# Kernel tuning notes

Measured on AMD Instinct MI355X. Metric: run time of the kernel, lower is better.

Reference implementation:

```python
import jax, jax.numpy as jnp
import numpy as np

N = 8192          # codeword length (power of 2)
K = 4096          # info bits (rate 1/2)
BS = 8192         # batch of codewords


def _gen_indices(n):
    """Stage-wise gather indices for the Arikan butterfly.
    Row s: position ind_dest XORs with ind_dest + 2**s; all other positions
    gather the sentinel column n, which holds a constant 0 (XOR identity)."""
    nb_stages = int(np.log2(n))
    ind = np.full((nb_stages, n + 1), n, dtype=np.int32)
    for s in range(nb_stages):
        r = np.arange(n // 2)
        ind_dest = r * 2 - (r % (2 ** s))
        ind[s, ind_dest] = ind_dest + 2 ** s
    return ind


def setup_inputs() -> dict:
    key = jax.random.key(0)
    u = jax.random.randint(key, (BS, K), 0, 2).astype(jnp.float32)  # info bits in {0,1}
    frozen_pos = np.arange(N - K)
    info_pos = jnp.asarray(np.setdiff1d(np.arange(N), frozen_pos), dtype=jnp.int32)
    ind_gather = jnp.asarray(_gen_indices(N))  # [log2(N), N+1] int32
    return {"u": u, "info_pos": info_pos, "ind_gather": ind_gather}


def reference(u, info_pos, ind_gather):
    bs = u.shape[0]
    n = ind_gather.shape[1] - 1
    nb_stages = ind_gather.shape[0]
    # scatter info bits into codeword positions (frozen positions stay 0)
    c = jnp.zeros((bs, n), dtype=u.dtype).at[:, info_pos].set(u)
    # append the zero sentinel column used as XOR identity
    x = jnp.concatenate([c, jnp.zeros((bs, 1), dtype=u.dtype)], axis=1)  # [bs, n+1]
    for s in range(nb_stages):  # fixed log2(n) structurally-distinct stages
        x = (x + x[:, ind_gather[s]]) % 2  # XOR on {0,1} bits
    return x[:, :n]
```

## Files before the change

kernel.cpp:

```cpp
#include <hip/hip_runtime.h>


typedef unsigned u32x4 __attribute__((ext_vector_type(4)));

constexpr int ROWS      = 8192;
constexpr int K_QUADS   = 1024;
constexpr int OUT_WORDS = 8192;

__global__ __launch_bounds__(64)
void polar_encode_kernel(const u32x4* __restrict__ u, unsigned* __restrict__ out) {
    __shared__ u32x4 lds[1024];

    const int l   = threadIdx.x;
    const int row = blockIdx.x;

    const u32x4* urow = u + (size_t)row * K_QUADS + (size_t)l * 16;
    u32x4 v[16];
#pragma unroll
    for (int r = 0; r < 16; ++r) v[r] = __builtin_nontemporal_load(&urow[r]);

#pragma unroll
    for (int r = 0; r < 16; ++r) { v[r][0] ^= v[r][1]; v[r][2] ^= v[r][3]; }
#pragma unroll
    for (int r = 0; r < 16; ++r) { v[r][0] ^= v[r][2]; v[r][1] ^= v[r][3]; }
#pragma unroll
    for (int s = 0; s < 4; ++s) {
#pragma unroll
        for (int r = 0; r < 16; ++r) {
            if (!(r & (1 << s))) {
                const int p = r | (1 << s);
                v[r][0] ^= v[p][0]; v[r][1] ^= v[p][1];
                v[r][2] ^= v[p][2]; v[r][3] ^= v[p][3];
            }
        }
    }

    const int swz = l & 15;
#pragma unroll
    for (int r = 0; r < 16; ++r)
        lds[(l << 4) + (r ^ swz)] = v[r];

    __syncthreads();

    const unsigned* ldsw = (const unsigned*)lds;
    const int cbase = l >> 2;
    const int clow  = l & 3;
    unsigned g[64];
#pragma unroll
    for (int j = 0; j < 64; ++j) {
        g[j] = ldsw[(j << 6) + ((cbase ^ (j & 15)) << 2) + clow];
    }

#pragma unroll
    for (int s = 0; s < 6; ++s) {
#pragma unroll
        for (int j = 0; j < 64; ++j) {
            if (!(j & (1 << s))) g[j] ^= g[j | (1 << s)];
        }
    }

    unsigned* orow = out + (size_t)row * OUT_WORDS;
#pragma unroll
    for (int j = 0; j < 64; ++j) {
        const int o = (j << 6) + l;
        __builtin_nontemporal_store(g[j], &orow[o]);
        __builtin_nontemporal_store(g[j], &orow[4096 + o]);
    }
}

extern "C" void kernel_launch(void* const* d_in, const int* in_sizes, int n_in,
                              void* d_out, int out_size, void* d_ws, size_t ws_size,
                              hipStream_t stream) {
    (void)in_sizes; (void)n_in; (void)d_ws; (void)ws_size; (void)out_size;
    const u32x4* u = (const u32x4*)d_in[0];
    unsigned* out = (unsigned*)d_out;

    hipLaunchKernelGGL(polar_encode_kernel, dim3(ROWS), dim3(64), 0, stream,
                       u, out);
}
```

Before: 389.2 us.

## Split each row across 256 threads with two LDS transpose passes

Each row is now encoded by 256 threads instead of 64. Every thread loads 4 coalesced quads, and the butterfly is split across two swizzled LDS transposes with an extra barrier. Register pressure falls sharply, from 64 words per thread to 16, so occupancy should rise, and the global loads and stores become coalesced. Nontemporal loads and stores are replaced by ordinary accesses. The cost is a second LDS round trip and more synchronization.

```diff
diff --git a/kernel.cpp b/kernel.cpp
--- a/kernel.cpp
+++ b/kernel.cpp
@@ -3,68 +3,78 @@
 
 typedef unsigned u32x4 __attribute__((ext_vector_type(4)));
 
-constexpr int ROWS      = 8192;
-constexpr int K_QUADS   = 1024;
-constexpr int OUT_WORDS = 8192;
+constexpr int ROWS = 8192;
 
-__global__ __launch_bounds__(64)
+__global__ __launch_bounds__(256, 8)
 void polar_encode_kernel(const u32x4* __restrict__ u, unsigned* __restrict__ out) {
-    __shared__ u32x4 lds[1024];
+    __shared__ u32x4 lds4[1024];
+    unsigned* lds = (unsigned*)lds4;
 
-    const int l   = threadIdx.x;
+    const int t   = threadIdx.x;
     const int row = blockIdx.x;
 
-    const u32x4* urow = u + (size_t)row * K_QUADS + (size_t)l * 16;
-    u32x4 v[16];
+    const u32x4* urow = u + (size_t)row * 1024;
+    u32x4 v[4];
 #pragma unroll
-    for (int r = 0; r < 16; ++r) v[r] = __builtin_nontemporal_load(&urow[r]);
+    for (int k = 0; k < 4; ++k) v[k] = urow[k * 256 + t];
 
 #pragma unroll
-    for (int r = 0; r < 16; ++r) { v[r][0] ^= v[r][1]; v[r][2] ^= v[r][3]; }
+    for (int k = 0; k < 4; ++k) {
+        v[k][0] ^= v[k][1]; v[k][2] ^= v[k][3];
+        v[k][0] ^= v[k][2]; v[k][1] ^= v[k][3];
+    }
+    v[0] ^= v[1]; v[2] ^= v[3];
+    v[0] ^= v[2]; v[1] ^= v[3];
+
 #pragma unroll
-    for (int r = 0; r < 16; ++r) { v[r][0] ^= v[r][2]; v[r][1] ^= v[r][3]; }
+    for (int k = 0; k < 4; ++k) {
+        const int qw = k * 256 + t;
+        lds4[qw ^ ((qw >> 4) & 15)] = v[k];
+    }
+    __syncthreads();
+
+    const int xsw   = (t >> 2) & 15;
+    const int qbase = ((t >> 6) << 8) | (xsw << 4);
+    const int cw    = t & 3;
+    unsigned h[16];
+#pragma unroll
+    for (int i = 0; i < 16; ++i)
+        h[i] = lds[(qbase + (i ^ xsw)) * 4 + cw];
+
 #pragma unroll
     for (int s = 0; s < 4; ++s) {
 #pragma unroll
-        for (int r = 0; r < 16; ++r) {
-            if (!(r & (1 << s))) {
-                const int p = r | (1 << s);
-                v[r][0] ^= v[p][0]; v[r][1] ^= v[p][1];
-                v[r][2] ^= v[p][2]; v[r][3] ^= v[p][3];
-            }
-        }
-    }
-
-    const int swz = l & 15;
-#pragma unroll
-    for (int r = 0; r < 16; ++r)
-        lds[(l << 4) + (r ^ swz)] = v[r];
-
-    __syncthreads();
-
-    const unsigned* ldsw = (const unsigned*)lds;
-    const int cbase = l >> 2;
-    const int clow  = l & 3;
-    unsigned g[64];
-#pragma unroll
-    for (int j = 0; j < 64; ++j) {
-        g[j] = ldsw[(j << 6) + ((cbase ^ (j & 15)) << 2) + clow];
+        for (int i = 0; i < 16; ++i)
+            if (!(i & (1 << s))) h[i] ^= h[i | (1 << s)];
     }
 
 #pragma unroll
-    for (int s = 0; s < 6; ++s) {
+    for (int i = 0; i < 16; ++i)
+        lds[(qbase + (i ^ xsw)) * 4 + cw] = h[i];
+    __syncthreads();
+
+    const int hi = (t >> 6) << 8;
+    unsigned o_[16];
 #pragma unroll
-        for (int j = 0; j < 64; ++j) {
-            if (!(j & (1 << s))) g[j] ^= g[j | (1 << s)];
-        }
+    for (int j = 0; j < 16; ++j) {
+        const int g2 = hi | (j << 4) | (xsw ^ j);
+        o_[j] = lds[g2 * 4 + cw];
     }
 
-    unsigned* orow = out + (size_t)row * OUT_WORDS;
 #pragma unroll
-    for (int j = 0; j < 64; ++j) {
-        const int o = (j << 6) + l;
-        __builtin_nontemporal_store(g[j], &orow[o]);
-        __builtin_nontemporal_store(g[j], &orow[4096 + o]);
+    for (int s = 0; s < 4; ++s) {
+#pragma unroll
+        for (int j = 0; j < 16; ++j)
+            if (!(j & (1 << s))) o_[j] ^= o_[j | (1 << s)];
+    }
+
+    unsigned* orow = out + (size_t)row * 8192;
+    const int wbase = ((t >> 6) << 10) | (t & 63);
+#pragma unroll
+    for (int j = 0; j < 16; ++j) {
+        const int w = wbase + (j << 6);
+        orow[w]        = o_[j];
+        orow[4096 + w] = o_[j];
     }
 }
 
@@ -75,6 +85,6 @@
     const u32x4* u = (const u32x4*)d_in[0];
     unsigned* out = (unsigned*)d_out;
 
-    hipLaunchKernelGGL(polar_encode_kernel, dim3(ROWS), dim3(64), 0, stream,
+    hipLaunchKernelGGL(polar_encode_kernel, dim3(ROWS), dim3(256), 0, stream,
                        u, out);
 }
```

Measured after the change: 359.4 us. 7.7% less time.
